# Performance work log

Hardware: AMD Instinct MI355X
Metric: run time of the kernel (lower is better)

Reference implementation:

```python
import jax, jax.numpy as jnp
from jax import lax
import numpy as np

B = 16384
D = 32
N_HEADS = 4


def _piece_table():
    base = np.zeros((7, 4, 4), np.int32)
    cells = [
        [(1, 0), (1, 1), (1, 2), (1, 3)],  # I
        [(1, 1), (1, 2), (2, 1), (2, 2)],  # O
        [(1, 1), (2, 0), (2, 1), (2, 2)],  # T
        [(1, 1), (1, 2), (2, 0), (2, 1)],  # S
        [(1, 0), (1, 1), (2, 1), (2, 2)],  # Z
        [(1, 0), (2, 0), (2, 1), (2, 2)],  # J
        [(1, 2), (2, 0), (2, 1), (2, 2)],  # L
    ]
    for i, cs in enumerate(cells):
        for (r, c) in cs:
            base[i, r, c] = 1
    rots = np.stack([np.stack([np.rot90(base[i], k) for k in range(4)]) for i in range(7)])
    p = np.concatenate([rots, np.zeros((1, 4, 4, 4), np.int32)], 0)  # [8,4,4,4]
    return jnp.asarray(p)


def setup_inputs() -> dict:
    key = jax.random.key(0)
    ks = jax.random.split(key, 24)

    def ri(k, n, lo, hi):
        return jax.random.randint(k, (B, n), lo, hi, dtype=jnp.int32)

    t = jnp.concatenate([
        ri(ks[0], 1, 0, 10),   # col0 feature
        ri(ks[1], 1, 2, 8),
        ri(ks[2], 1, 0, 10),   # col2 y pos
        ri(ks[3], 1, 0, 8),    # col3 drop dist
        ri(ks[4], 1, 0, 4),    # col4 rotation
        ri(ks[5], 3, 0, 10),   # cols5-7
        ri(ks[6], 1, 0, 7),    # col8 piece id
        ri(ks[7], 6, 0, 7),    # cols9-14 hold/next
        ri(ks[8], 7, 0, 10),   # cols15-21
        ri(ks[9], 210, 0, 2),  # cols22-231 board
    ], axis=1)

    s = 0.05
    rn = lambda k, shp: jax.random.normal(k, shp, jnp.float32) * s
    return {
        "t": t,
        "piece_table": _piece_table(),
        "conv1_w": rn(ks[10], (6, 3, 5, 5)), "conv1_b": rn(ks[11], (6,)),
        "conv2_w": rn(ks[12], (16, 6, 5, 5)), "conv2_b": rn(ks[13], (16,)),
        "conv3_w": rn(ks[14], (64, 16, 3, 1)), "conv3_b": rn(ks[15], (64,)),
        "lfc1_w": rn(ks[16], (32, 64)), "lfc1_b": rn(ks[17], (32,)),
        "fc_w": rn(ks[18], (32, 8)), "fc_b": rn(ks[19], (32,)),
        "emb": rn(ks[20], (8, D)),
        "in_proj_w": rn(ks[21], (3 * D, D)), "in_proj_b": jnp.zeros((3 * D,), jnp.float32),
        "out_proj_w": rn(ks[22], (D, D)), "out_proj_b": jnp.zeros((D,), jnp.float32),
    }


def _avgpool2(x):
    b, c, h, w = x.shape
    h2, w2 = h // 2, w // 2
    return x[:, :, :h2 * 2, :w2 * 2].reshape(b, c, h2, 2, w2, 2).mean((3, 5))


def _lenet(x, w1, b1, w2, b2, w3, b3, fw, fb):
    dn = ("NCHW", "OIHW", "NCHW")
    x = jax.nn.relu(lax.conv_general_dilated(x, w1, (1, 1), ((2, 2), (2, 2)), dimension_numbers=dn) + b1[None, :, None, None])
    x = _avgpool2(x)                                   # [B,6,11,6]
    x = jax.nn.relu(lax.conv_general_dilated(x, w2, (1, 1), ((0, 0), (0, 0)), dimension_numbers=dn) + b2[None, :, None, None])
    x = _avgpool2(x)                                   # [B,16,3,1]
    x = jax.nn.relu(lax.conv_general_dilated(x, w3, (1, 1), ((0, 0), (0, 0)), dimension_numbers=dn) + b3[None, :, None, None])
    x = x.reshape(-1, 64)
    return jax.nn.relu(x @ fw.T + fb)                  # [B,32]


def _pe():
    pos = jnp.array([0, 0, 1, 2, 3, 4, 5], jnp.float32)[:, None]
    div = jnp.exp(jnp.arange(0, D, 2, dtype=jnp.float32) * (-jnp.log(10000.0) / D))
    s, c = jnp.sin(pos * div), jnp.cos(pos * div)      # [7,16] each
    return jnp.stack([s, c], -1).reshape(7, D)         # interleaved sin/cos


def _mha(q_in, kv, in_w, in_b, out_w, out_b):
    qw, kw, vw = in_w[:D], in_w[D:2 * D], in_w[2 * D:]
    qb, kb, vb = in_b[:D], in_b[D:2 * D], in_b[2 * D:]
    b, lq, _ = q_in.shape
    hd = D // N_HEADS
    q = (q_in @ qw.T + qb).reshape(b, lq, N_HEADS, hd)
    k = (kv @ kw.T + kb).reshape(b, -1, N_HEADS, hd)
    v = (kv @ vw.T + vb).reshape(b, -1, N_HEADS, hd)
    scores = jnp.einsum("bqhd,bkhd->bhqk", q, k) / jnp.sqrt(jnp.float32(hd))
    w = jax.nn.softmax(scores, axis=-1)
    o = jnp.einsum("bhqk,bkhd->bqhd", w, v).reshape(b, lq, D)
    return o @ out_w.T + out_b


def reference(t, piece_table, conv1_w, conv1_b, conv2_w, conv2_b, conv3_w, conv3_b,
              lfc1_w, lfc1_b, fc_w, fc_b, emb, in_proj_w, in_proj_b, out_proj_w, out_proj_b):
    bsz = t.shape[0]
    board = jnp.zeros((bsz, 3, 21, 10), jnp.float32)
    board = board.at[:, 0].set(t[:, 22:232].astype(jnp.float32).reshape(bsz, 21, 10))

    # gather piece grid, extract the 4 filled cells per sample in row-major order
    pieces = piece_table[t[:, 8], t[:, 4]].reshape(bsz, 16)        # [B,16] in {0,1}
    idx = jnp.argsort(1 - pieces, axis=1, stable=True)[:, :4]      # first 4 ones, scan order
    cy, cx = idx // 4, idx % 4
    x = cx + t[:, 1][:, None] - 2
    y = cy + t[:, 2][:, None]
    ny = y + t[:, 3][:, None]
    mask = (y >= 0) & (ny >= 0)
    br = jnp.arange(bsz, dtype=jnp.int32)[:, None]
    y_m = jnp.where(mask, y, -1)
    ny_m = jnp.where(mask, ny, -1)
    board = board.at[br, 1, y_m, x].set(1.0, mode="drop")
    board = board.at[br, 2, ny_m, x].set(1.0, mode="drop")

    board = jnp.pad(board, ((0, 0), (0, 0), (0, 1), (1, 1)), constant_values=1.0)  # [B,3,22,12]

    t9 = jnp.where((t[:, 9] != -1) & (t[:, 6] != 0), t[:, 9], 7)
    hold_next = jnp.concatenate([t[:, 8:9], t9[:, None], t[:, 10:15]], axis=1)     # [B,7]

    b2 = _lenet(board, conv1_w, conv1_b, conv2_w, conv2_b, conv3_w, conv3_b, lfc1_w, lfc1_b)  # [B,32]
    bkv = b2[:, None, :]                                            # [B,1,32]
    p = emb[hold_next] + _pe()[None]                                # [B,7,32]
    a = _mha(p, bkv, in_proj_w, in_proj_b, out_proj_w, out_proj_b)  # [B,7,32]

    xf = jax.nn.relu(t[:, :8].astype(jnp.float32) @ fc_w.T + fc_b)  # [B,32]
    out = jnp.concatenate([xf, a.mean(axis=1), b2], axis=1)         # [B,96]
    return (out, board)
```

## Files before the change

kernel.cpp:

```cpp
#include <hip/hip_runtime.h>
#include <cstddef>


#define BATCH 16384
#define SPB   4
#define NBLK  (BATCH / SPB)
#define RS    18
#define P1OFF  432
#define PCSOFF 800
#define SS2    816

#define BSYNC() asm volatile("s_waitcnt lgkmcnt(0)\ns_barrier" ::: "memory")

static __device__ __forceinline__ float dot4(float4 a, float4 b) {
  return a.x * b.x + a.y * b.y + a.z * b.z + a.w * b.w;
}

__global__ __launch_bounds__(256)
void cb8_kernel(const float* __restrict__ w1, float* __restrict__ cb8)
{
  int i = blockIdx.x * 256 + threadIdx.x;
  if (i >= 2112) return;
  int p = i >> 3, o = i & 7;
  float acc = 0.f;
  if (o < 6) {
    int y0 = p / 12, x0 = p - y0 * 12;
#pragma unroll
    for (int dy = 0; dy < 5; ++dy)
#pragma unroll
      for (int dx = 0; dx < 5; ++dx) {
        int pr = y0 + dy - 2, pc = x0 + dx - 2;
        if (pr >= 0 && pr < 22 && pc >= 0 && pc < 12 &&
            (pr == 21 || pc == 0 || pc == 11)) {
          int k = dy * 5 + dx;
          acc += w1[(o * 3 + 0) * 25 + k] + w1[(o * 3 + 1) * 25 + k]
               + w1[(o * 3 + 2) * 25 + k];
        }
      }
  }
  cb8[i] = acc;
}

__global__ __launch_bounds__(256, 4)
void board_model_kernel(const int* __restrict__ t,
                        const int* __restrict__ piece_table,
                        const float* __restrict__ w1, const float* __restrict__ b1,
                        const float* __restrict__ w2, const float* __restrict__ b2w,
                        const float* __restrict__ w3, const float* __restrict__ b3,
                        const float* __restrict__ wf1, const float* __restrict__ bf1,
                        const float* __restrict__ fcw, const float* __restrict__ fcb,
                        const float* __restrict__ ipw, const float* __restrict__ ipb,
                        const float* __restrict__ opw, const float* __restrict__ opb,
                        const float* __restrict__ cbg,
                        float* __restrict__ out,
                        float* __restrict__ out_board)
{
  __shared__ __align__(16) float scr[SPB * SS2];
  __shared__ float w1L[300];

  const int tid  = threadIdx.x;
  const int lane = tid & 63;
  const int wv   = tid >> 6;
  const int bb   = blockIdx.x * SPB;

  for (int i = tid; i < 300; i += 256) {
    int o = i % 6, tt = i / 6, m = tt / 25, tp = tt - m * 25;
    w1L[i] = w1[(o * 3 + m + 1) * 25 + tp];
  }

  {
    float* W = &scr[wv * SS2];
    int*   pcs = (int*)&scr[wv * SS2 + PCSOFF];
    int*   bmi = (int*)&scr[wv * SS2 + P1OFF];
    const int* tr = t + (size_t)(bb + wv) * 232;

    float4* W4 = (float4*)W;
    for (int i = lane; i < 108; i += 64) W4[i] = float4{0.f, 0.f, 0.f, 0.f};
    if (lane < 44) bmi[lane] = 0;

    {
      const int2* cp = (const int2*)(tr + 22);
      for (int v = lane; v < 105; v += 64) {
        int2 cv = cp[v];
        int i0 = v * 2;
        int r = i0 / 10, b = i0 - r * 10;
        W[(r + 2) * RS + b + 5] = (float)cv.x;
        W[(r + 2) * RS + b + 6] = (float)cv.y;
      }
    }

    {
      const int* pt = piece_table + (tr[8] * 4 + tr[4]) * 16;
      int ptv = (lane < 16) ? pt[lane] : 0;
      unsigned long long bal = __ballot(ptv != 0);
      if (lane < 4) {
        unsigned x = (unsigned)bal & 0xffffu;
        for (int k = 0; k < lane; ++k) x &= x - 1;
        int sel = __builtin_ctz(x);
        int cy = sel >> 2, cx = sel & 3;
        int xx = cx + tr[1] - 2;
        int y  = cy + tr[2];
        int ny = y + tr[3];
        bool mask = (y >= 0) && (ny >= 0);
        bool xok  = (xx >= 0) && (xx < 10);
        bool v1 = mask && xok && (y < 21);
        bool v2 = mask && xok && (ny < 21);
        pcs[2 * lane + 0]       = v1 ? y  : -100;
        pcs[2 * lane + 1]       = xx + 1;
        pcs[2 * (lane + 4)]     = v2 ? ny : -100;
        pcs[2 * (lane + 4) + 1] = xx + 1;
        if (v1) atomicOr(&bmi[y],       1 << (xx + 1));
        if (v2) atomicOr(&bmi[22 + ny], 1 << (xx + 1));
      }
    }
    __builtin_amdgcn_wave_barrier();

    float* ob = out_board + (size_t)(bb + wv) * 792;
    for (int v = lane; v < 198; v += 64) {
      int ch = v / 66, w = v - ch * 66;
      int r = w / 3, c = (w - r * 3) * 4;
      float val[4];
      if (ch == 0) {
#pragma unroll
        for (int d = 0; d < 4; ++d) {
          int cd = c + d;
          val[d] = (r == 21 || cd == 0 || cd == 11) ? 1.f
                 : W[(r + 2) * RS + cd + 4];
        }
      } else {
        int bits = bmi[(ch - 1) * 22 + r];
#pragma unroll
        for (int d = 0; d < 4; ++d) {
          int cd = c + d;
          val[d] = (r == 21 || cd == 0 || cd == 11 || ((bits >> cd) & 1)) ? 1.f : 0.f;
        }
      }
      *(float4*)(ob + v * 4) = float4{val[0], val[1], val[2], val[3]};
    }
  }
  BSYNC();

  if (lane < 60) {
    int p = lane;
    int r = p / 6, c = p - r * 6;
    const float* Wq  = &scr[wv * SS2];
    const int*   pcs = (const int*)&scr[wv * SS2 + PCSOFF];

    float acc[2][2][6];
#pragma unroll
    for (int i = 0; i < 2; ++i)
#pragma unroll
      for (int j = 0; j < 2; ++j) {
        int pcell = (2 * r + i) * 12 + (2 * c + j);
        float4 ca  = *(const float4*)(cbg + pcell * 8);
        float2 ca2 = *(const float2*)(cbg + pcell * 8 + 4);
        acc[i][j][0] = b1[0] + ca.x;  acc[i][j][1] = b1[1] + ca.y;
        acc[i][j][2] = b1[2] + ca.z;  acc[i][j][3] = b1[3] + ca.w;
        acc[i][j][4] = b1[4] + ca2.x; acc[i][j][5] = b1[5] + ca2.y;
      }

#pragma unroll 1
    for (int u = 0; u < 6; ++u) {
      const float* base = Wq + (2 * r + u) * RS + (2 * c + 2);
      float2 a0 = *(const float2*)(base);
      float2 a1 = *(const float2*)(base + 2);
      float2 a2 = *(const float2*)(base + 4);
      float rv[6] = {a0.x, a0.y, a1.x, a1.y, a2.x, a2.y};
#pragma unroll
      for (int i = 0; i < 2; ++i) {
        int ky = u - i;
        if (ky < 0 || ky > 4) continue;
#pragma unroll
        for (int j = 0; j < 2; ++j)
#pragma unroll
          for (int kx = 0; kx < 5; ++kx) {
            float xv = rv[j + kx];
#pragma unroll
            for (int o = 0; o < 6; ++o)
              acc[i][j][o] += xv * w1[o * 75 + ky * 5 + kx];
          }
      }
    }

#pragma unroll 1
    for (int e = 0; e < 8; ++e) {
      int pr = pcs[2 * e];
      if (pr < 0) continue;
      int pc = pcs[2 * e + 1];
      int chm = e >> 2;
      int dyb = pr + 2 - 2 * r;
      int dxb = pc + 2 - 2 * c;
      if (dyb < 0 || dyb > 5 || dxb < 0 || dxb > 5) continue;
#pragma unroll
      for (int i = 0; i < 2; ++i) {
        int dy = dyb - i;
        if ((unsigned)dy >= 5u) continue;
#pragma unroll
        for (int j = 0; j < 2; ++j) {
          int dx = dxb - j;
          if ((unsigned)dx >= 5u) continue;
          const float* wp = &w1L[(chm * 25 + dy * 5 + dx) * 6];
#pragma unroll
          for (int o = 0; o < 6; ++o)
            acc[i][j][o] += wp[o];
        }
      }
    }

    float* P1q = &scr[wv * SS2 + P1OFF];
#pragma unroll
    for (int o = 0; o < 6; ++o) {
      float v = fmaxf(acc[0][0][o], 0.f) + fmaxf(acc[0][1][o], 0.f)
              + fmaxf(acc[1][0][o], 0.f) + fmaxf(acc[1][1][o], 0.f);
      P1q[o * 61 + p] = 0.25f * v;
    }
  }
  BSYNC();

  const int wvu = __builtin_amdgcn_readfirstlane(wv);

  if (lane < 48) {
    int q = lane / 12, p = lane - q * 12;
    int r = p >> 1, c = p & 1;
    const float* P1q = &scr[q * SS2 + P1OFF];
    float a4[4];
#pragma unroll
    for (int oo = 0; oo < 4; ++oo) a4[oo] = b2w[4 * wvu + oo];

#pragma unroll 1
    for (int ic = 0; ic < 6; ++ic) {
      const float* pb = P1q + ic * 61 + r * 6 + c;
      const float* wp = w2 + (size_t)(4 * wvu) * 150 + ic * 25;
#pragma unroll 1
      for (int kr = 0; kr < 5; ++kr) {
        float x0 = pb[kr * 6 + 0];
        float x1 = pb[kr * 6 + 1];
        float x2 = pb[kr * 6 + 2];
        float x3 = pb[kr * 6 + 3];
        float x4 = pb[kr * 6 + 4];
        const float* wr = wp + kr * 5;
#pragma unroll
        for (int oo = 0; oo < 4; ++oo) {
          const float* w = wr + oo * 150;
          a4[oo] += x0 * w[0] + x1 * w[1] + x2 * w[2] + x3 * w[3] + x4 * w[4];
        }
      }
    }
    float* C2q = &scr[q * SS2];
#pragma unroll
    for (int oo = 0; oo < 4; ++oo)
      C2q[(4 * wvu + oo) * 12 + p] = fmaxf(a4[oo], 0.f);
  }
  BSYNC();

  {
    const int q = wvu;
    float* S = &scr[q * SS2];

    if (lane < 48) {
      int o = lane / 3, pr = lane - o * 3;
      float4 v4 = *(const float4*)(S + o * 12 + 4 * pr);
      S[192 + lane] = 0.25f * (v4.x + v4.y + v4.z + v4.w);
    }
    __builtin_amdgcn_wave_barrier();

    {
      int o = lane;
      const float4* w34 = (const float4*)(w3 + o * 48);
      const float4* S4  = (const float4*)(S + 192);
      float acc = b3[o];
#pragma unroll 1
      for (int m = 0; m < 12; ++m)
        acc += dot4(S4[m], w34[m]);
      S[240 + o] = fmaxf(acc, 0.f);
    }
    __builtin_amdgcn_wave_barrier();

    {
      int j = lane & 31, h = lane >> 5;
      const float4* wf4 = (const float4*)(wf1 + j * 64 + 32 * h);
      const float4* S4  = (const float4*)(S + 240 + 32 * h);
      float part = 0.f;
#pragma unroll 1
      for (int m = 0; m < 8; ++m)
        part += dot4(S4[m], wf4[m]);
      part += __shfl_xor(part, 32, 64);
      if (h == 0) {
        float acc = fmaxf(bf1[j] + part, 0.f);
        S[304 + j] = acc;
        out[(size_t)(bb + q) * 96 + 64 + j] = acc;
      }
    }
    __builtin_amdgcn_wave_barrier();

    {
      int j = lane & 31;
      if (lane < 32) {
        const float4* ip4 = (const float4*)(ipw + (size_t)(64 + j) * 32);
        const float4* S4  = (const float4*)(S + 304);
        float acc = ipb[64 + j];
#pragma unroll 1
        for (int m = 0; m < 8; ++m)
          acc += dot4(S4[m], ip4[m]);
        S[336 + j] = acc;
      } else {
        const int4* t4 = (const int4*)(t + (size_t)(bb + q) * 232);
        int4 ta = t4[0], tb = t4[1];
        const float4* fc4 = (const float4*)(fcw + j * 8);
        float4 wa = fc4[0], wb = fc4[1];
        float acc = fcb[j]
                  + (float)ta.x * wa.x + (float)ta.y * wa.y
                  + (float)ta.z * wa.z + (float)ta.w * wa.w
                  + (float)tb.x * wb.x + (float)tb.y * wb.y
                  + (float)tb.z * wb.z + (float)tb.w * wb.w;
        out[(size_t)(bb + q) * 96 + j] = fmaxf(acc, 0.f);
      }
    }
    __builtin_amdgcn_wave_barrier();

    if (lane < 32) {
      int j = lane;
      const float4* op4 = (const float4*)(opw + j * 32);
      const float4* S4  = (const float4*)(S + 336);
      float acc = opb[j];
#pragma unroll 1
      for (int m = 0; m < 8; ++m)
        acc += dot4(S4[m], op4[m]);
      out[(size_t)(bb + q) * 96 + 32 + j] = acc;
    }
  }
}

extern "C" void kernel_launch(void* const* d_in, const int* in_sizes, int n_in,
                              void* d_out, int out_size, void* d_ws, size_t ws_size,
                              hipStream_t stream) {
  const int*   t   = (const int*)d_in[0];
  const int*   pt  = (const int*)d_in[1];
  const float* w1  = (const float*)d_in[2];
  const float* b1  = (const float*)d_in[3];
  const float* w2  = (const float*)d_in[4];
  const float* b2w = (const float*)d_in[5];
  const float* w3  = (const float*)d_in[6];
  const float* b3  = (const float*)d_in[7];
  const float* wf1 = (const float*)d_in[8];
  const float* bf1 = (const float*)d_in[9];
  const float* fcw = (const float*)d_in[10];
  const float* fcb = (const float*)d_in[11];
  const float* ipw = (const float*)d_in[13];
  const float* ipb = (const float*)d_in[14];
  const float* opw = (const float*)d_in[15];
  const float* opb = (const float*)d_in[16];

  float* out       = (float*)d_out;
  float* out_board = out + (size_t)BATCH * 96;
  float* cbg       = (float*)d_ws;

  hipLaunchKernelGGL(cb8_kernel, dim3(9), dim3(256), 0, stream, w1, cbg);
  hipLaunchKernelGGL(board_model_kernel, dim3(NBLK), dim3(256), 0, stream,
                     t, pt, w1, b1, w2, b2w, w3, b3, wf1, bf1, fcw, fcb,
                     ipw, ipb, opw, opb, cbg, out, out_board);
}
```

Before: 183.0 us.

## Pre-transpose conv weights in prep kernel and use packed f2 FMA for convolutions

The prep kernel now also writes transposed conv1 and conv2 weight layouts into the workspace and folds the conv1 bias into the border correction table. The conv1 and conv2 inner loops then accumulate with two-wide float vectors so the compiler can emit packed FMA instructions, and they read the transposed weights as contiguous pairs. This targets scalar weight loads and ALU issue count in the convolution stages. In exchange, one extra small pre-kernel pass runs and the weights come from the global workspace.

```diff
diff --git a/kernel.cpp b/kernel.cpp
--- a/kernel.cpp
+++ b/kernel.cpp
@@ -10,35 +10,53 @@
 #define PCSOFF 800
 #define SS2    816
 
+#define WS_CB   0
+#define WS_W1D  2112
+#define WS_W2T  2272
+#define WS_TOT  4672
+
 #define BSYNC() asm volatile("s_waitcnt lgkmcnt(0)\ns_barrier" ::: "memory")
+
+typedef float f2 __attribute__((ext_vector_type(2)));
 
 static __device__ __forceinline__ float dot4(float4 a, float4 b) {
   return a.x * b.x + a.y * b.y + a.z * b.z + a.w * b.w;
 }
 
 __global__ __launch_bounds__(256)
-void cb8_kernel(const float* __restrict__ w1, float* __restrict__ cb8)
+void prep_kernel(const float* __restrict__ w1, const float* __restrict__ b1,
+                 const float* __restrict__ w2, float* __restrict__ ws)
 {
   int i = blockIdx.x * 256 + threadIdx.x;
-  if (i >= 2112) return;
-  int p = i >> 3, o = i & 7;
-  float acc = 0.f;
-  if (o < 6) {
-    int y0 = p / 12, x0 = p - y0 * 12;
-#pragma unroll
-    for (int dy = 0; dy < 5; ++dy)
-#pragma unroll
-      for (int dx = 0; dx < 5; ++dx) {
-        int pr = y0 + dy - 2, pc = x0 + dx - 2;
-        if (pr >= 0 && pr < 22 && pc >= 0 && pc < 12 &&
-            (pr == 21 || pc == 0 || pc == 11)) {
-          int k = dy * 5 + dx;
-          acc += w1[(o * 3 + 0) * 25 + k] + w1[(o * 3 + 1) * 25 + k]
-               + w1[(o * 3 + 2) * 25 + k];
-        }
-      }
-  }
-  cb8[i] = acc;
+  if (i < 2112) {
+    int p = i >> 3, o = i & 7;
+    float acc = 0.f;
+    if (o < 6) {
+      acc = b1[o];
+      int y0 = p / 12, x0 = p - y0 * 12;
+#pragma unroll
+      for (int dy = 0; dy < 5; ++dy)
+#pragma unroll
+        for (int dx = 0; dx < 5; ++dx) {
+          int pr = y0 + dy - 2, pc = x0 + dx - 2;
+          if (pr >= 0 && pr < 22 && pc >= 0 && pc < 12 &&
+              (pr == 21 || pc == 0 || pc == 11)) {
+            int k = dy * 5 + dx;
+            acc += w1[(o * 3 + 0) * 25 + k] + w1[(o * 3 + 1) * 25 + k]
+                 + w1[(o * 3 + 2) * 25 + k];
+          }
+        }
+    }
+    ws[WS_CB + i] = acc;
+  } else if (i < WS_W1D + 150) {
+    int idx = i - WS_W1D;
+    int tap = idx / 6, o = idx - tap * 6;
+    ws[i] = w1[o * 75 + tap];
+  } else if (i >= WS_W2T && i < WS_TOT) {
+    int idx = i - WS_W2T;
+    int tap = idx >> 4, o = idx & 15;
+    ws[i] = w2[o * 150 + tap];
+  }
 }
 
 __global__ __launch_bounds__(256, 4)
@@ -56,7 +74,7 @@
                         float* __restrict__ out_board)
 {
   __shared__ __align__(16) float scr[SPB * SS2];
-  __shared__ float w1L[300];
+  __shared__ __align__(16) float w1L[300];
 
   const int tid  = threadIdx.x;
   const int lane = tid & 63;
@@ -145,8 +163,9 @@
     int r = p / 6, c = p - r * 6;
     const float* Wq  = &scr[wv * SS2];
     const int*   pcs = (const int*)&scr[wv * SS2 + PCSOFF];
-
-    float acc[2][2][6];
+    const float* w1d = cbg + WS_W1D;
+
+    f2 acc2[2][2][3];
 #pragma unroll
     for (int i = 0; i < 2; ++i)
 #pragma unroll
@@ -154,18 +173,18 @@
         int pcell = (2 * r + i) * 12 + (2 * c + j);
         float4 ca  = *(const float4*)(cbg + pcell * 8);
         float2 ca2 = *(const float2*)(cbg + pcell * 8 + 4);
-        acc[i][j][0] = b1[0] + ca.x;  acc[i][j][1] = b1[1] + ca.y;
-        acc[i][j][2] = b1[2] + ca.z;  acc[i][j][3] = b1[3] + ca.w;
-        acc[i][j][4] = b1[4] + ca2.x; acc[i][j][5] = b1[5] + ca2.y;
+        acc2[i][j][0] = f2{ca.x, ca.y};
+        acc2[i][j][1] = f2{ca.z, ca.w};
+        acc2[i][j][2] = f2{ca2.x, ca2.y};
       }
 
 #pragma unroll 1
     for (int u = 0; u < 6; ++u) {
       const float* base = Wq + (2 * r + u) * RS + (2 * c + 2);
-      float2 a0 = *(const float2*)(base);
-      float2 a1 = *(const float2*)(base + 2);
-      float2 a2 = *(const float2*)(base + 4);
-      float rv[6] = {a0.x, a0.y, a1.x, a1.y, a2.x, a2.y};
+      float2 q0 = *(const float2*)(base);
+      float2 q1 = *(const float2*)(base + 2);
+      float2 q2 = *(const float2*)(base + 4);
+      float rv[6] = {q0.x, q0.y, q1.x, q1.y, q2.x, q2.y};
 #pragma unroll
       for (int i = 0; i < 2; ++i) {
         int ky = u - i;
@@ -175,9 +194,11 @@
 #pragma unroll
           for (int kx = 0; kx < 5; ++kx) {
             float xv = rv[j + kx];
-#pragma unroll
-            for (int o = 0; o < 6; ++o)
-              acc[i][j][o] += xv * w1[o * 75 + ky * 5 + kx];
+            const f2* wp = (const f2*)(w1d + (ky * 5 + kx) * 6);
+            f2 xb = {xv, xv};
+            acc2[i][j][0] += xb * wp[0];
+            acc2[i][j][1] += xb * wp[1];
+            acc2[i][j][2] += xb * wp[2];
           }
       }
     }
@@ -199,20 +220,28 @@
         for (int j = 0; j < 2; ++j) {
           int dx = dxb - j;
           if ((unsigned)dx >= 5u) continue;
-          const float* wp = &w1L[(chm * 25 + dy * 5 + dx) * 6];
-#pragma unroll
-          for (int o = 0; o < 6; ++o)
-            acc[i][j][o] += wp[o];
+          const f2* wp = (const f2*)(&w1L[(chm * 25 + dy * 5 + dx) * 6]);
+          acc2[i][j][0] += wp[0];
+          acc2[i][j][1] += wp[1];
+          acc2[i][j][2] += wp[2];
         }
       }
     }
 
     float* P1q = &scr[wv * SS2 + P1OFF];
 #pragma unroll
-    for (int o = 0; o < 6; ++o) {
-      float v = fmaxf(acc[0][0][o], 0.f) + fmaxf(acc[0][1][o], 0.f)
-              + fmaxf(acc[1][0][o], 0.f) + fmaxf(acc[1][1][o], 0.f);
-      P1q[o * 61 + p] = 0.25f * v;
+    for (int k = 0; k < 3; ++k) {
+      f2 s = {0.f, 0.f};
+#pragma unroll
+      for (int i = 0; i < 2; ++i)
+#pragma unroll
+        for (int j = 0; j < 2; ++j) {
+          f2 v = acc2[i][j][k];
+          s.x += fmaxf(v.x, 0.f);
+          s.y += fmaxf(v.y, 0.f);
+        }
+      P1q[(2 * k + 0) * 61 + p] = 0.25f * s.x;
+      P1q[(2 * k + 1) * 61 + p] = 0.25f * s.y;
     }
   }
   BSYNC();
@@ -223,33 +252,31 @@
     int q = lane / 12, p = lane - q * 12;
     int r = p >> 1, c = p & 1;
     const float* P1q = &scr[q * SS2 + P1OFF];
-    float a4[4];
-#pragma unroll
-    for (int oo = 0; oo < 4; ++oo) a4[oo] = b2w[4 * wvu + oo];
+    const float* w2T = cbg + WS_W2T + 4 * wvu;
+    float4 bw = *(const float4*)(b2w + 4 * wvu);
+    f2 a20 = {bw.x, bw.y};
+    f2 a21 = {bw.z, bw.w};
 
 #pragma unroll 1
     for (int ic = 0; ic < 6; ++ic) {
       const float* pb = P1q + ic * 61 + r * 6 + c;
-      const float* wp = w2 + (size_t)(4 * wvu) * 150 + ic * 25;
 #pragma unroll 1
       for (int kr = 0; kr < 5; ++kr) {
-        float x0 = pb[kr * 6 + 0];
-        float x1 = pb[kr * 6 + 1];
-        float x2 = pb[kr * 6 + 2];
-        float x3 = pb[kr * 6 + 3];
-        float x4 = pb[kr * 6 + 4];
-        const float* wr = wp + kr * 5;
-#pragma unroll
-        for (int oo = 0; oo < 4; ++oo) {
-          const float* w = wr + oo * 150;
-          a4[oo] += x0 * w[0] + x1 * w[1] + x2 * w[2] + x3 * w[3] + x4 * w[4];
+#pragma unroll
+        for (int kc = 0; kc < 5; ++kc) {
+          float xv = pb[kr * 6 + kc];
+          const f2* wp = (const f2*)(w2T + (size_t)(ic * 25 + kr * 5 + kc) * 16);
+          f2 xb = {xv, xv};
+          a20 += xb * wp[0];
+          a21 += xb * wp[1];
         }
       }
     }
     float* C2q = &scr[q * SS2];
-#pragma unroll
-    for (int oo = 0; oo < 4; ++oo)
-      C2q[(4 * wvu + oo) * 12 + p] = fmaxf(a4[oo], 0.f);
+    C2q[(4 * wvu + 0) * 12 + p] = fmaxf(a20.x, 0.f);
+    C2q[(4 * wvu + 1) * 12 + p] = fmaxf(a20.y, 0.f);
+    C2q[(4 * wvu + 2) * 12 + p] = fmaxf(a21.x, 0.f);
+    C2q[(4 * wvu + 3) * 12 + p] = fmaxf(a21.y, 0.f);
   }
   BSYNC();
 
@@ -355,7 +382,7 @@
   float* out_board = out + (size_t)BATCH * 96;
   float* cbg       = (float*)d_ws;
 
-  hipLaunchKernelGGL(cb8_kernel, dim3(9), dim3(256), 0, stream, w1, cbg);
+  hipLaunchKernelGGL(prep_kernel, dim3(19), dim3(256), 0, stream, w1, b1, w2, cbg);
   hipLaunchKernelGGL(board_model_kernel, dim3(NBLK), dim3(256), 0, stream,
                      t, pt, w1, b1, w2, b2w, w3, b3, wf1, bf1, fcw, fcb,
                      ipw, ipb, opw, opb, cbg, out, out_board);
```

New measurement: 183.3 us. About the same (+0.2%).
